# Kernel tuning notes

Hardware: AMD Instinct MI355X
Metric: run time of the kernel (lower is better)

The kernel has to match this reference:

```python
import jax, jax.numpy as jnp
import numpy as np

MARGIN = 1.0
EPS = 1e-8  # torch F.cosine_similarity default eps


def setup_inputs() -> dict:
    key = jax.random.key(0)
    k1, k2 = jax.random.split(key)
    reps = jax.random.normal(k1, (8192, 512), dtype=jnp.float32)
    labels = jax.random.randint(k2, (8192,), 0, 100, dtype=jnp.int64)
    return {"reps": reps, "labels": labels}


def reference(reps, labels):
    # cosine_similarity(reps[None, :, :], reps[:, None, :], dim=2)
    # == dot(a,b) / (max(||a||,eps) * max(||b||,eps)); compute via normalize + GEMM
    norms = jnp.maximum(jnp.linalg.norm(reps, axis=1, keepdims=True), EPS)
    xn = reps / norms  # [N, D]
    cos_sim = xn @ xn.T  # [N, N]
    label_matrix = labels[None, :] == labels[:, None]  # [N, N] bool
    same_class_loss = jnp.where(label_matrix, (1.0 - cos_sim) ** 2, 0.0)
    diff_class_loss = jnp.where(label_matrix, 0.0,
                                jnp.maximum(MARGIN - cos_sim, 0.0) ** 2)
    loss = same_class_loss + diff_class_loss
    return loss.mean()
```

## Files before the change

kernel.cpp:

```cpp
#include <hip/hip_runtime.h>


typedef __attribute__((ext_vector_type(8))) short  s8;
typedef __attribute__((ext_vector_type(8))) __bf16 bf8;
typedef __attribute__((ext_vector_type(4))) float  f4;

#define NT32 136
#define KOUT 16
#define KCW  512
#define GSTRIDE (256 * 512)

#define OFF_XT  0u
#define OFF_S2  (8u * 1024u * 1024u)
#define OFF_TK  (OFF_S2 + 4u)
#define OFF_PRT (OFF_S2 + 64u)
#define OFF_GP  (OFF_PRT + 256u * 512u * 4u)

__device__ __forceinline__ unsigned short f2bf(float f) {
    union { float f; unsigned u; } v; v.f = f;
    unsigned r = v.u + 0x7FFFu + ((v.u >> 16) & 1u);
    return (unsigned short)(r >> 16);
}
__device__ __forceinline__ float bf2f(unsigned short h) {
    union { unsigned u; float f; } v; v.u = ((unsigned)h) << 16;
    return v.f;
}

__global__ __launch_bounds__(256) void k_prep(
    const float* __restrict__ reps, unsigned short* __restrict__ xt,
    float* __restrict__ parts, float* __restrict__ s2, int* __restrict__ ticket)
{
    __shared__ unsigned short tile[32][528];
    const int t = threadIdx.x, lane = t & 63, wv = t >> 6;
    const int b = blockIdx.x;
    if (b == 0 && t == 0) { *s2 = 0.f; *ticket = 0; }

    const int row = wv * 8 + (lane >> 3);
    const int co  = (lane & 7) * 4;
    const float* rp = reps + (size_t)(b * 32 + row) * 512 + co;
    float4 v[16];
    float ss = 0.f;
    #pragma unroll
    for (int q = 0; q < 16; ++q) {
        v[q] = *(const float4*)(rp + 32 * q);
        ss += v[q].x*v[q].x + v[q].y*v[q].y + v[q].z*v[q].z + v[q].w*v[q].w;
    }
    ss += __shfl_xor(ss, 1, 64);
    ss += __shfl_xor(ss, 2, 64);
    ss += __shfl_xor(ss, 4, 64);
    const float inv = 1.0f / fmaxf(sqrtf(ss), 1e-8f);
    #pragma unroll
    for (int q = 0; q < 16; ++q) {
        ushort4 p;
        p.x = f2bf(v[q].x * inv); p.y = f2bf(v[q].y * inv);
        p.z = f2bf(v[q].z * inv); p.w = f2bf(v[q].w * inv);
        *(ushort4*)&tile[row][co + 32 * q] = p;
    }
    __syncthreads();

    {
        const int rl = lane & 15, ks = lane >> 4;
        #pragma unroll
        for (int gg = 0; gg < 8; ++gg) {
            const int g = wv * 8 + gg;
            const int a = g * 16 + rl;
            ushort4 o0, o1;
            o0.x = tile[ks*8+0][a]; o0.y = tile[ks*8+1][a];
            o0.z = tile[ks*8+2][a]; o0.w = tile[ks*8+3][a];
            o1.x = tile[ks*8+4][a]; o1.y = tile[ks*8+5][a];
            o1.z = tile[ks*8+6][a]; o1.w = tile[ks*8+7][a];
            unsigned short* dst = xt + ((size_t)g << 17) + ((size_t)b << 9) + lane * 8;
            *(ushort4*)(dst)     = o0;
            *(ushort4*)(dst + 4) = o1;
        }
    }

    {
        float sA = 0.f, sB = 0.f;
        #pragma unroll
        for (int r = 0; r < 32; ++r) {
            sA += bf2f(tile[r][t]);
            sB += bf2f(tile[r][t + 256]);
        }
        parts[(size_t)b * 512 + t]       = sA;
        parts[(size_t)b * 512 + t + 256] = sB;
    }
}

__global__ __launch_bounds__(64) void k_gram(
    const unsigned short* __restrict__ xt, float* __restrict__ gp)
{
    const int lane = threadIdx.x;
    const int l15 = lane & 15, l4 = lane >> 4;
    int tt = blockIdx.x, ta = 0;
    while (tt >= 16 - ta) { tt -= 16 - ta; ++ta; }
    const int tb = ta + tt;
    const int c0 = blockIdx.y * (KCW / 32);
    const unsigned short* A0 = xt + (((size_t)(ta * 2) * 256 + c0) << 9) + lane * 8;
    const unsigned short* B0 = xt + (((size_t)(tb * 2) * 256 + c0) << 9) + lane * 8;

    f4 acc00 = {0.f,0.f,0.f,0.f}, acc01 = {0.f,0.f,0.f,0.f};
    f4 acc10 = {0.f,0.f,0.f,0.f}, acc11 = {0.f,0.f,0.f,0.f};

    if (ta != tb) {
        for (int cc = 0; cc < 16; ++cc) {
            const s8 av0 = *(const s8*)(A0 + cc * 512);
            const s8 av1 = *(const s8*)(A0 + GSTRIDE + cc * 512);
            const s8 bv0 = *(const s8*)(B0 + cc * 512);
            const s8 bv1 = *(const s8*)(B0 + GSTRIDE + cc * 512);
            acc00 = __builtin_amdgcn_mfma_f32_16x16x32_bf16(
                __builtin_bit_cast(bf8, av0), __builtin_bit_cast(bf8, bv0), acc00, 0, 0, 0);
            acc01 = __builtin_amdgcn_mfma_f32_16x16x32_bf16(
                __builtin_bit_cast(bf8, av0), __builtin_bit_cast(bf8, bv1), acc01, 0, 0, 0);
            acc10 = __builtin_amdgcn_mfma_f32_16x16x32_bf16(
                __builtin_bit_cast(bf8, av1), __builtin_bit_cast(bf8, bv0), acc10, 0, 0, 0);
            acc11 = __builtin_amdgcn_mfma_f32_16x16x32_bf16(
                __builtin_bit_cast(bf8, av1), __builtin_bit_cast(bf8, bv1), acc11, 0, 0, 0);
        }
    } else {
        for (int cc = 0; cc < 16; ++cc) {
            const s8 av0 = *(const s8*)(A0 + cc * 512);
            const s8 av1 = *(const s8*)(A0 + GSTRIDE + cc * 512);
            acc00 = __builtin_amdgcn_mfma_f32_16x16x32_bf16(
                __builtin_bit_cast(bf8, av0), __builtin_bit_cast(bf8, av0), acc00, 0, 0, 0);
            acc01 = __builtin_amdgcn_mfma_f32_16x16x32_bf16(
                __builtin_bit_cast(bf8, av0), __builtin_bit_cast(bf8, av1), acc01, 0, 0, 0);
            acc10 = __builtin_amdgcn_mfma_f32_16x16x32_bf16(
                __builtin_bit_cast(bf8, av1), __builtin_bit_cast(bf8, av0), acc10, 0, 0, 0);
            acc11 = __builtin_amdgcn_mfma_f32_16x16x32_bf16(
                __builtin_bit_cast(bf8, av1), __builtin_bit_cast(bf8, av1), acc11, 0, 0, 0);
        }
    }

    float* gb = gp + ((size_t)blockIdx.y * NT32 + blockIdx.x) * 1024;
    #pragma unroll
    for (int r = 0; r < 4; ++r) {
        const int ar0 = (l4 * 4 + r) * 32 + l15;
        gb[ar0]           = acc00[r];
        gb[ar0 + 16]      = acc01[r];
        gb[ar0 + 16 * 32] = acc10[r];
        gb[ar0 + 16 * 33] = acc11[r];
    }
}

__global__ __launch_bounds__(256) void k_reduce_final(
    const float* __restrict__ gp, const float* __restrict__ parts,
    float* __restrict__ s2, int* __restrict__ ticket, float* __restrict__ out)
{
    __shared__ float part[4], svp[4];
    __shared__ int lastFlag;
    const int t = threadIdx.x, lane = t & 63, wv = t >> 6;
    const int c = blockIdx.x * 256 + t;
    const f4* g4 = (const f4*)gp;
    f4 s = {0.f, 0.f, 0.f, 0.f};
    #pragma unroll
    for (int p = 0; p < KOUT; ++p) s += g4[(size_t)p * (NT32 * 256) + c];
    int tt = c >> 8, ta = 0;
    while (tt >= 16 - ta) { tt -= 16 - ta; ++ta; }
    const float wgt = (tt == 0) ? 1.f : 2.f;
    float sq = wgt * (s.x * s.x + s.y * s.y + s.z * s.z + s.w * s.w);
    #pragma unroll
    for (int off = 1; off < 64; off <<= 1) sq += __shfl_xor(sq, off, 64);
    if (lane == 0) part[wv] = sq;

    float sv = 0.f;
    if (blockIdx.x < 128) {
        const int a = blockIdx.x * 4 + wv;
        #pragma unroll
        for (int pb = 0; pb < 4; ++pb) sv += parts[(size_t)(pb * 64 + lane) * 512 + a];
        #pragma unroll
        for (int off = 1; off < 64; off <<= 1) sv += __shfl_xor(sv, off, 64);
    }
    if (lane == 0) svp[wv] = sv;
    __syncthreads();
    if (t == 0) {
        const float tot = part[0] + part[1] + part[2] + part[3]
            - 2.f * (svp[0]*svp[0] + svp[1]*svp[1] + svp[2]*svp[2] + svp[3]*svp[3]);
        atomicAdd(s2, tot);
        __threadfence();
        lastFlag = (atomicAdd(ticket, 1) == (int)gridDim.x - 1);
    }
    __syncthreads();
    if (lastFlag) {
        __threadfence();
        if (t == 0) {
            const float S = atomicAdd(s2, 0.f);
            const double NN = 67108864.0;
            out[0] = (float)((NN + (double)S) / NN);
        }
    }
}

extern "C" void kernel_launch(void* const* d_in, const int* in_sizes, int n_in,
                              void* d_out, int out_size, void* d_ws, size_t ws_size,
                              hipStream_t stream)
{
    const float* reps = (const float*)d_in[0];
    char* ws = (char*)d_ws;
    unsigned short* xt   = (unsigned short*)(ws + OFF_XT);
    float*          s2   = (float*)(ws + OFF_S2);
    int*            tick = (int*)(ws + OFF_TK);
    float*          prt  = (float*)(ws + OFF_PRT);
    float*          gp   = (float*)(ws + OFF_GP);

    k_prep<<<256, 256, 0, stream>>>(reps, xt, prt, s2, tick);
    k_gram<<<dim3(NT32, KOUT), 64, 0, stream>>>(xt, gp);
    k_reduce_final<<<NT32, 256, 0, stream>>>(gp, prt, s2, tick, (float*)d_out);
}
```

Measured before the change: 87.33 us.

## Split prep into more blocks and move column sums into reduce kernel

The prep kernel now uses 1024 blocks of 8 rows each instead of 256 blocks of 32 rows, which raises parallelism and shrinks shared memory per block. It no longer writes per-block column partial sums. The reduce kernel grows to 272 Gram-reduction blocks, each splitting the 16 K-planes across two thread halves, plus 32 extra blocks that recompute the column sums by reading the bf16 transposed matrix. This spreads the work across more blocks in both kernels, at the cost of re-reading the 8 MB bf16 buffer in the final kernel.

```diff
diff --git a/kernel.cpp b/kernel.cpp
--- a/kernel.cpp
+++ b/kernel.cpp
@@ -9,12 +9,14 @@
 #define KOUT 16
 #define KCW  512
 #define GSTRIDE (256 * 512)
+#define PLANE_F4 (NT32 * 256)
+#define RBLK 272
+#define SBLK 32
 
 #define OFF_XT  0u
 #define OFF_S2  (8u * 1024u * 1024u)
 #define OFF_TK  (OFF_S2 + 4u)
-#define OFF_PRT (OFF_S2 + 64u)
-#define OFF_GP  (OFF_PRT + 256u * 512u * 4u)
+#define OFF_GP  (OFF_S2 + 64u)
 
 __device__ __forceinline__ unsigned short f2bf(float f) {
     union { float f; unsigned u; } v; v.f = f;
@@ -28,62 +30,48 @@
 
 __global__ __launch_bounds__(256) void k_prep(
     const float* __restrict__ reps, unsigned short* __restrict__ xt,
-    float* __restrict__ parts, float* __restrict__ s2, int* __restrict__ ticket)
-{
-    __shared__ unsigned short tile[32][528];
-    const int t = threadIdx.x, lane = t & 63, wv = t >> 6;
+    float* __restrict__ s2, int* __restrict__ ticket)
+{
+    __shared__ unsigned short tile[8][528];
+    const int t = threadIdx.x;
     const int b = blockIdx.x;
     if (b == 0 && t == 0) { *s2 = 0.f; *ticket = 0; }
-
-    const int row = wv * 8 + (lane >> 3);
-    const int co  = (lane & 7) * 4;
-    const float* rp = reps + (size_t)(b * 32 + row) * 512 + co;
-    float4 v[16];
+    const int c = b >> 2, ks = b & 3;
+    const int j = t >> 5;
+    const int cl = t & 31;
+
+    const float* rp = reps + (size_t)(c * 32 + ks * 8 + j) * 512 + cl * 4;
+    float4 v[4];
     float ss = 0.f;
     #pragma unroll
-    for (int q = 0; q < 16; ++q) {
-        v[q] = *(const float4*)(rp + 32 * q);
+    for (int q = 0; q < 4; ++q) {
+        v[q] = *(const float4*)(rp + q * 128);
         ss += v[q].x*v[q].x + v[q].y*v[q].y + v[q].z*v[q].z + v[q].w*v[q].w;
     }
-    ss += __shfl_xor(ss, 1, 64);
-    ss += __shfl_xor(ss, 2, 64);
-    ss += __shfl_xor(ss, 4, 64);
+    ss += __shfl_xor(ss, 1, 64);  ss += __shfl_xor(ss, 2, 64);
+    ss += __shfl_xor(ss, 4, 64);  ss += __shfl_xor(ss, 8, 64);
+    ss += __shfl_xor(ss, 16, 64);
     const float inv = 1.0f / fmaxf(sqrtf(ss), 1e-8f);
     #pragma unroll
-    for (int q = 0; q < 16; ++q) {
+    for (int q = 0; q < 4; ++q) {
         ushort4 p;
         p.x = f2bf(v[q].x * inv); p.y = f2bf(v[q].y * inv);
         p.z = f2bf(v[q].z * inv); p.w = f2bf(v[q].w * inv);
-        *(ushort4*)&tile[row][co + 32 * q] = p;
+        *(ushort4*)&tile[j][cl * 4 + q * 128] = p;
     }
     __syncthreads();
 
-    {
-        const int rl = lane & 15, ks = lane >> 4;
-        #pragma unroll
-        for (int gg = 0; gg < 8; ++gg) {
-            const int g = wv * 8 + gg;
-            const int a = g * 16 + rl;
-            ushort4 o0, o1;
-            o0.x = tile[ks*8+0][a]; o0.y = tile[ks*8+1][a];
-            o0.z = tile[ks*8+2][a]; o0.w = tile[ks*8+3][a];
-            o1.x = tile[ks*8+4][a]; o1.y = tile[ks*8+5][a];
-            o1.z = tile[ks*8+6][a]; o1.w = tile[ks*8+7][a];
-            unsigned short* dst = xt + ((size_t)g << 17) + ((size_t)b << 9) + lane * 8;
-            *(ushort4*)(dst)     = o0;
-            *(ushort4*)(dst + 4) = o1;
-        }
-    }
-
-    {
-        float sA = 0.f, sB = 0.f;
-        #pragma unroll
-        for (int r = 0; r < 32; ++r) {
-            sA += bf2f(tile[r][t]);
-            sB += bf2f(tile[r][t + 256]);
-        }
-        parts[(size_t)b * 512 + t]       = sA;
-        parts[(size_t)b * 512 + t + 256] = sB;
+    #pragma unroll
+    for (int s_ = 0; s_ < 2; ++s_) {
+        const int a = t + s_ * 256;
+        const int g = a >> 4, rl = a & 15;
+        ushort4 o0, o1;
+        o0.x = tile[0][a]; o0.y = tile[1][a]; o0.z = tile[2][a]; o0.w = tile[3][a];
+        o1.x = tile[4][a]; o1.y = tile[5][a]; o1.z = tile[6][a]; o1.w = tile[7][a];
+        unsigned short* dst = xt + ((size_t)g << 17) + ((size_t)c << 9)
+                                 + (ks * 16 + rl) * 8;
+        *(ushort4*)(dst)     = o0;
+        *(ushort4*)(dst + 4) = o1;
     }
 }
 
@@ -144,50 +132,74 @@
 }
 
 __global__ __launch_bounds__(256) void k_reduce_final(
-    const float* __restrict__ gp, const float* __restrict__ parts,
+    const float* __restrict__ gp, const unsigned short* __restrict__ xt,
     float* __restrict__ s2, int* __restrict__ ticket, float* __restrict__ out)
 {
-    __shared__ float part[4], svp[4];
+    __shared__ f4 sh[128];
+    __shared__ float pw[4];
     __shared__ int lastFlag;
     const int t = threadIdx.x, lane = t & 63, wv = t >> 6;
-    const int c = blockIdx.x * 256 + t;
-    const f4* g4 = (const f4*)gp;
-    f4 s = {0.f, 0.f, 0.f, 0.f};
-    #pragma unroll
-    for (int p = 0; p < KOUT; ++p) s += g4[(size_t)p * (NT32 * 256) + c];
-    int tt = c >> 8, ta = 0;
-    while (tt >= 16 - ta) { tt -= 16 - ta; ++ta; }
-    const float wgt = (tt == 0) ? 1.f : 2.f;
-    float sq = wgt * (s.x * s.x + s.y * s.y + s.z * s.z + s.w * s.w);
-    #pragma unroll
-    for (int off = 1; off < 64; off <<= 1) sq += __shfl_xor(sq, off, 64);
-    if (lane == 0) part[wv] = sq;
-
-    float sv = 0.f;
-    if (blockIdx.x < 128) {
-        const int a = blockIdx.x * 4 + wv;
+    const int bx = blockIdx.x;
+
+    if (bx < RBLK) {
+        const int cl = bx * 128 + (t & 127);
+        const int h = t >> 7;
+        const f4* g4 = (const f4*)gp;
+        f4 s = {0.f, 0.f, 0.f, 0.f};
         #pragma unroll
-        for (int pb = 0; pb < 4; ++pb) sv += parts[(size_t)(pb * 64 + lane) * 512 + a];
-        #pragma unroll
-        for (int off = 1; off < 64; off <<= 1) sv += __shfl_xor(sv, off, 64);
-    }
-    if (lane == 0) svp[wv] = sv;
+        for (int p = 0; p < 8; ++p) s += g4[(size_t)(h * 8 + p) * PLANE_F4 + cl];
+        if (h) sh[t & 127] = s;
+        __syncthreads();
+        float sq = 0.f;
+        if (!h) {
+            const f4 tot = s + sh[t];
+            int tt = cl >> 8, ta = 0;
+            while (tt >= 16 - ta) { tt -= 16 - ta; ++ta; }
+            const float wgt = (tt == 0) ? 1.f : 2.f;
+            sq = wgt * (tot.x*tot.x + tot.y*tot.y + tot.z*tot.z + tot.w*tot.w);
+            #pragma unroll
+            for (int off = 1; off < 64; off <<= 1) sq += __shfl_xor(sq, off, 64);
+        }
+        if (!h && lane == 0) pw[wv] = sq;
+        __syncthreads();
+        if (t == 0) {
+            atomicAdd(s2, pw[0] + pw[1]);
+            __threadfence();
+            lastFlag = (atomicAdd(ticket, 1) == (int)gridDim.x - 1);
+        }
+    } else {
+        const int g = bx - RBLK;
+        const unsigned short* base = xt + ((size_t)g << 17) + lane * 8;
+        float acc = 0.f;
+        for (int c = wv * 64; c < wv * 64 + 64; ++c) {
+            const ushort4 u0 = *(const ushort4*)(base + ((size_t)c << 9));
+            const ushort4 u1 = *(const ushort4*)(base + ((size_t)c << 9) + 4);
+            acc += bf2f(u0.x) + bf2f(u0.y) + bf2f(u0.z) + bf2f(u0.w)
+                 + bf2f(u1.x) + bf2f(u1.y) + bf2f(u1.z) + bf2f(u1.w);
+        }
+        acc += __shfl_xor(acc, 16, 64);
+        acc += __shfl_xor(acc, 32, 64);
+        if (lane < 16) ((float*)sh)[wv * 16 + lane] = acc;
+        __syncthreads();
+        if (t < 16) {
+            const float* svp = (const float*)sh;
+            const float sa = svp[t] + svp[16 + t] + svp[32 + t] + svp[48 + t];
+            float q = sa * sa;
+            q += __shfl_xor(q, 1, 64); q += __shfl_xor(q, 2, 64);
+            q += __shfl_xor(q, 4, 64); q += __shfl_xor(q, 8, 64);
+            if (t == 0) {
+                atomicAdd(s2, -2.f * q);
+                __threadfence();
+                lastFlag = (atomicAdd(ticket, 1) == (int)gridDim.x - 1);
+            }
+        }
+    }
     __syncthreads();
-    if (t == 0) {
-        const float tot = part[0] + part[1] + part[2] + part[3]
-            - 2.f * (svp[0]*svp[0] + svp[1]*svp[1] + svp[2]*svp[2] + svp[3]*svp[3]);
-        atomicAdd(s2, tot);
+    if (lastFlag && t == 0) {
         __threadfence();
-        lastFlag = (atomicAdd(ticket, 1) == (int)gridDim.x - 1);
-    }
-    __syncthreads();
-    if (lastFlag) {
-        __threadfence();
-        if (t == 0) {
-            const float S = atomicAdd(s2, 0.f);
-            const double NN = 67108864.0;
-            out[0] = (float)((NN + (double)S) / NN);
-        }
+        const float S = atomicAdd(s2, 0.f);
+        const double NN = 67108864.0;
+        out[0] = (float)((NN + (double)S) / NN);
     }
 }
 
@@ -200,10 +212,9 @@
     unsigned short* xt   = (unsigned short*)(ws + OFF_XT);
     float*          s2   = (float*)(ws + OFF_S2);
     int*            tick = (int*)(ws + OFF_TK);
-    float*          prt  = (float*)(ws + OFF_PRT);
     float*          gp   = (float*)(ws + OFF_GP);
 
-    k_prep<<<256, 256, 0, stream>>>(reps, xt, prt, s2, tick);
+    k_prep<<<1024, 256, 0, stream>>>(reps, xt, s2, tick);
     k_gram<<<dim3(NT32, KOUT), 64, 0, stream>>>(xt, gp);
-    k_reduce_final<<<NT32, 256, 0, stream>>>(gp, prt, s2, tick, (float*)d_out);
-}
+    k_reduce_final<<<RBLK + SBLK, 256, 0, stream>>>(gp, xt, s2, tick, (float*)d_out);
+}
```

Measured after the change: 104.8 us. 20.0% more time.

## Fuse gram computation and reduction into one kernel with in-block K split

Applied to the files above, without the earlier changes.

Merges the split-K gram kernel and the reduction kernel into a single launch. Each block's four waves split the K dimension and reduce their partial tiles through shared memory, so the global partial buffer is no longer written and read back. Extra blocks compute the column-sum correction term, and a ticket counter finalizes the result. Fewer waves now run longer serial MFMA chains, which may reduce parallelism and latency hiding.

```diff
diff --git a/kernel.cpp b/kernel.cpp
--- a/kernel.cpp
+++ b/kernel.cpp
@@ -5,16 +5,14 @@
 typedef __attribute__((ext_vector_type(8))) __bf16 bf8;
 typedef __attribute__((ext_vector_type(4))) float  f4;
 
-#define NT32 136
-#define KOUT 16
-#define KCW  512
+#define TILES 136
+#define SVB   128
 #define GSTRIDE (256 * 512)
 
 #define OFF_XT  0u
 #define OFF_S2  (8u * 1024u * 1024u)
 #define OFF_TK  (OFF_S2 + 4u)
 #define OFF_PRT (OFF_S2 + 64u)
-#define OFF_GP  (OFF_PRT + 256u * 512u * 4u)
 
 __device__ __forceinline__ unsigned short f2bf(float f) {
     union { float f; unsigned u; } v; v.f = f;
@@ -87,103 +85,97 @@
     }
 }
 
-__global__ __launch_bounds__(64) void k_gram(
-    const unsigned short* __restrict__ xt, float* __restrict__ gp)
-{
-    const int lane = threadIdx.x;
-    const int l15 = lane & 15, l4 = lane >> 4;
-    int tt = blockIdx.x, ta = 0;
-    while (tt >= 16 - ta) { tt -= 16 - ta; ++ta; }
-    const int tb = ta + tt;
-    const int c0 = blockIdx.y * (KCW / 32);
-    const unsigned short* A0 = xt + (((size_t)(ta * 2) * 256 + c0) << 9) + lane * 8;
-    const unsigned short* B0 = xt + (((size_t)(tb * 2) * 256 + c0) << 9) + lane * 8;
-
-    f4 acc00 = {0.f,0.f,0.f,0.f}, acc01 = {0.f,0.f,0.f,0.f};
-    f4 acc10 = {0.f,0.f,0.f,0.f}, acc11 = {0.f,0.f,0.f,0.f};
-
-    if (ta != tb) {
-        for (int cc = 0; cc < 16; ++cc) {
-            const s8 av0 = *(const s8*)(A0 + cc * 512);
-            const s8 av1 = *(const s8*)(A0 + GSTRIDE + cc * 512);
-            const s8 bv0 = *(const s8*)(B0 + cc * 512);
-            const s8 bv1 = *(const s8*)(B0 + GSTRIDE + cc * 512);
-            acc00 = __builtin_amdgcn_mfma_f32_16x16x32_bf16(
-                __builtin_bit_cast(bf8, av0), __builtin_bit_cast(bf8, bv0), acc00, 0, 0, 0);
-            acc01 = __builtin_amdgcn_mfma_f32_16x16x32_bf16(
-                __builtin_bit_cast(bf8, av0), __builtin_bit_cast(bf8, bv1), acc01, 0, 0, 0);
-            acc10 = __builtin_amdgcn_mfma_f32_16x16x32_bf16(
-                __builtin_bit_cast(bf8, av1), __builtin_bit_cast(bf8, bv0), acc10, 0, 0, 0);
-            acc11 = __builtin_amdgcn_mfma_f32_16x16x32_bf16(
-                __builtin_bit_cast(bf8, av1), __builtin_bit_cast(bf8, bv1), acc11, 0, 0, 0);
-        }
-    } else {
-        for (int cc = 0; cc < 16; ++cc) {
-            const s8 av0 = *(const s8*)(A0 + cc * 512);
-            const s8 av1 = *(const s8*)(A0 + GSTRIDE + cc * 512);
-            acc00 = __builtin_amdgcn_mfma_f32_16x16x32_bf16(
-                __builtin_bit_cast(bf8, av0), __builtin_bit_cast(bf8, av0), acc00, 0, 0, 0);
-            acc01 = __builtin_amdgcn_mfma_f32_16x16x32_bf16(
-                __builtin_bit_cast(bf8, av0), __builtin_bit_cast(bf8, av1), acc01, 0, 0, 0);
-            acc10 = __builtin_amdgcn_mfma_f32_16x16x32_bf16(
-                __builtin_bit_cast(bf8, av1), __builtin_bit_cast(bf8, av0), acc10, 0, 0, 0);
-            acc11 = __builtin_amdgcn_mfma_f32_16x16x32_bf16(
-                __builtin_bit_cast(bf8, av1), __builtin_bit_cast(bf8, av1), acc11, 0, 0, 0);
-        }
-    }
-
-    float* gb = gp + ((size_t)blockIdx.y * NT32 + blockIdx.x) * 1024;
-    #pragma unroll
-    for (int r = 0; r < 4; ++r) {
-        const int ar0 = (l4 * 4 + r) * 32 + l15;
-        gb[ar0]           = acc00[r];
-        gb[ar0 + 16]      = acc01[r];
-        gb[ar0 + 16 * 32] = acc10[r];
-        gb[ar0 + 16 * 33] = acc11[r];
-    }
-}
-
-__global__ __launch_bounds__(256) void k_reduce_final(
-    const float* __restrict__ gp, const float* __restrict__ parts,
+__global__ __launch_bounds__(256) void k_gram_final(
+    const unsigned short* __restrict__ xt, const float* __restrict__ parts,
     float* __restrict__ s2, int* __restrict__ ticket, float* __restrict__ out)
 {
-    __shared__ float part[4], svp[4];
-    __shared__ int lastFlag;
+    __shared__ float sh[4][1024];
+    __shared__ float pw[4];
     const int t = threadIdx.x, lane = t & 63, wv = t >> 6;
-    const int c = blockIdx.x * 256 + t;
-    const f4* g4 = (const f4*)gp;
-    f4 s = {0.f, 0.f, 0.f, 0.f};
-    #pragma unroll
-    for (int p = 0; p < KOUT; ++p) s += g4[(size_t)p * (NT32 * 256) + c];
-    int tt = c >> 8, ta = 0;
-    while (tt >= 16 - ta) { tt -= 16 - ta; ++ta; }
-    const float wgt = (tt == 0) ? 1.f : 2.f;
-    float sq = wgt * (s.x * s.x + s.y * s.y + s.z * s.z + s.w * s.w);
-    #pragma unroll
-    for (int off = 1; off < 64; off <<= 1) sq += __shfl_xor(sq, off, 64);
-    if (lane == 0) part[wv] = sq;
+    const int bx = blockIdx.x;
+    float contrib = 0.f;
 
-    float sv = 0.f;
-    if (blockIdx.x < 128) {
-        const int a = blockIdx.x * 4 + wv;
+    if (bx < TILES) {
+        const int l15 = lane & 15, l4 = lane >> 4;
+        int tt = bx, ta = 0;
+        while (tt >= 16 - ta) { tt -= 16 - ta; ++ta; }
+        const int tb = ta + tt;
+        const int c0 = wv * 64;
+        const unsigned short* A0 = xt + (((size_t)(ta * 2) * 256 + c0) << 9) + lane * 8;
+        const unsigned short* B0 = xt + (((size_t)(tb * 2) * 256 + c0) << 9) + lane * 8;
+
+        f4 acc00 = {0.f,0.f,0.f,0.f}, acc01 = {0.f,0.f,0.f,0.f};
+        f4 acc10 = {0.f,0.f,0.f,0.f}, acc11 = {0.f,0.f,0.f,0.f};
+
+        if (ta != tb) {
+            #pragma unroll 4
+            for (int cc = 0; cc < 64; ++cc) {
+                const s8 av0 = *(const s8*)(A0 + cc * 512);
+                const s8 av1 = *(const s8*)(A0 + GSTRIDE + cc * 512);
+                const s8 bv0 = *(const s8*)(B0 + cc * 512);
+                const s8 bv1 = *(const s8*)(B0 + GSTRIDE + cc * 512);
+                acc00 = __builtin_amdgcn_mfma_f32_16x16x32_bf16(
+                    __builtin_bit_cast(bf8, av0), __builtin_bit_cast(bf8, bv0), acc00, 0, 0, 0);
+                acc01 = __builtin_amdgcn_mfma_f32_16x16x32_bf16(
+                    __builtin_bit_cast(bf8, av0), __builtin_bit_cast(bf8, bv1), acc01, 0, 0, 0);
+                acc10 = __builtin_amdgcn_mfma_f32_16x16x32_bf16(
+                    __builtin_bit_cast(bf8, av1), __builtin_bit_cast(bf8, bv0), acc10, 0, 0, 0);
+                acc11 = __builtin_amdgcn_mfma_f32_16x16x32_bf16(
+                    __builtin_bit_cast(bf8, av1), __builtin_bit_cast(bf8, bv1), acc11, 0, 0, 0);
+            }
+        } else {
+            #pragma unroll 4
+            for (int cc = 0; cc < 64; ++cc) {
+                const s8 av0 = *(const s8*)(A0 + cc * 512);
+                const s8 av1 = *(const s8*)(A0 + GSTRIDE + cc * 512);
+                acc00 = __builtin_amdgcn_mfma_f32_16x16x32_bf16(
+                    __builtin_bit_cast(bf8, av0), __builtin_bit_cast(bf8, av0), acc00, 0, 0, 0);
+                acc01 = __builtin_amdgcn_mfma_f32_16x16x32_bf16(
+                    __builtin_bit_cast(bf8, av0), __builtin_bit_cast(bf8, av1), acc01, 0, 0, 0);
+                acc10 = __builtin_amdgcn_mfma_f32_16x16x32_bf16(
+                    __builtin_bit_cast(bf8, av1), __builtin_bit_cast(bf8, av0), acc10, 0, 0, 0);
+                acc11 = __builtin_amdgcn_mfma_f32_16x16x32_bf16(
+                    __builtin_bit_cast(bf8, av1), __builtin_bit_cast(bf8, av1), acc11, 0, 0, 0);
+            }
+        }
+
+        #pragma unroll
+        for (int r = 0; r < 4; ++r) {
+            const int row0 = l4 * 4 + r;
+            sh[wv][row0 * 32 + l15]             = acc00[r];
+            sh[wv][row0 * 32 + 16 + l15]        = acc01[r];
+            sh[wv][(16 + row0) * 32 + l15]      = acc10[r];
+            sh[wv][(16 + row0) * 32 + 16 + l15] = acc11[r];
+        }
+        __syncthreads();
+
+        f4 tot = {0.f, 0.f, 0.f, 0.f};
+        #pragma unroll
+        for (int w = 0; w < 4; ++w) tot += *(const f4*)&sh[w][t * 4];
+        const float wgt = (ta == tb) ? 1.f : 2.f;
+        float sq = wgt * (tot.x*tot.x + tot.y*tot.y + tot.z*tot.z + tot.w*tot.w);
+        #pragma unroll
+        for (int off = 1; off < 64; off <<= 1) sq += __shfl_xor(sq, off, 64);
+        if (lane == 0) pw[wv] = sq;
+        __syncthreads();
+        contrib = pw[0] + pw[1] + pw[2] + pw[3];
+    } else {
+        const int a = (bx - TILES) * 4 + wv;
+        float sv = 0.f;
         #pragma unroll
         for (int pb = 0; pb < 4; ++pb) sv += parts[(size_t)(pb * 64 + lane) * 512 + a];
         #pragma unroll
         for (int off = 1; off < 64; off <<= 1) sv += __shfl_xor(sv, off, 64);
+        if (lane == 0) pw[wv] = sv;
+        __syncthreads();
+        contrib = -2.f * (pw[0]*pw[0] + pw[1]*pw[1] + pw[2]*pw[2] + pw[3]*pw[3]);
     }
-    if (lane == 0) svp[wv] = sv;
-    __syncthreads();
+
     if (t == 0) {
-        const float tot = part[0] + part[1] + part[2] + part[3]
-            - 2.f * (svp[0]*svp[0] + svp[1]*svp[1] + svp[2]*svp[2] + svp[3]*svp[3]);
-        atomicAdd(s2, tot);
+        atomicAdd(s2, contrib);
         __threadfence();
-        lastFlag = (atomicAdd(ticket, 1) == (int)gridDim.x - 1);
-    }
-    __syncthreads();
-    if (lastFlag) {
-        __threadfence();
-        if (t == 0) {
+        if (atomicAdd(ticket, 1) == (int)gridDim.x - 1) {
+            __threadfence();
             const float S = atomicAdd(s2, 0.f);
             const double NN = 67108864.0;
             out[0] = (float)((NN + (double)S) / NN);
@@ -201,9 +193,7 @@
     float*          s2   = (float*)(ws + OFF_S2);
     int*            tick = (int*)(ws + OFF_TK);
     float*          prt  = (float*)(ws + OFF_PRT);
-    float*          gp   = (float*)(ws + OFF_GP);
 
     k_prep<<<256, 256, 0, stream>>>(reps, xt, prt, s2, tick);
-    k_gram<<<dim3(NT32, KOUT), 64, 0, stream>>>(xt, gp);
-    k_reduce_final<<<NT32, 256, 0, stream>>>(gp, prt, s2, tick, (float*)d_out);
+    k_gram_final<<<TILES + SVB, 256, 0, stream>>>(xt, prt, s2, tick, (float*)d_out);
 }
```

New measurement: 94.75 us. 1.08x slower.
